# Optimization experiments

Hardware: AMD Instinct MI355X
Metric: run time of the kernel (lower is better)

The kernel has to match this reference:

```python
import jax, jax.numpy as jnp
import numpy as np

D_MODEL = 1024
NUM_HEADS = 16
D_K = D_MODEL // NUM_HEADS
D_FF = 4096
THETA = 10000.0
EPS = 1e-5


def rmsnorm(x, w):
    ms = jnp.mean(jnp.square(x), axis=-1, keepdims=True)
    return x * jax.lax.rsqrt(ms + EPS) * w


def rope(x, pos):
    # x: [B, H, S, d_k]; pos: [S]
    half = x.shape[-1] // 2
    inv_freq = THETA ** (-jnp.arange(half, dtype=x.dtype) * 2.0 / x.shape[-1])  # [half]
    ang = pos.astype(x.dtype)[:, None] * inv_freq[None, :]  # [S, half]
    cos, sin = jnp.cos(ang), jnp.sin(ang)
    xe, xo = x[..., 0::2], x[..., 1::2]
    oe = xe * cos - xo * sin
    oo = xe * sin + xo * cos
    return jnp.stack([oe, oo], axis=-1).reshape(x.shape)


def setup_inputs() -> dict:
    key = jax.random.key(0)
    ks = jax.random.split(key, 10)
    std_d = 1.0 / np.sqrt(D_MODEL)
    std_f = 1.0 / np.sqrt(D_FF)
    B, S = 4, 2048
    return {
        "x": jax.random.normal(ks[0], (B, S, D_MODEL), dtype=jnp.float32),
        "token_positions": jnp.arange(S, dtype=jnp.int32),
        "q_proj": jax.random.normal(ks[1], (D_MODEL, D_MODEL), dtype=jnp.float32) * std_d,
        "k_proj": jax.random.normal(ks[2], (D_MODEL, D_MODEL), dtype=jnp.float32) * std_d,
        "v_proj": jax.random.normal(ks[3], (D_MODEL, D_MODEL), dtype=jnp.float32) * std_d,
        "o_proj": jax.random.normal(ks[4], (D_MODEL, D_MODEL), dtype=jnp.float32) * std_d,
        "w1": jax.random.normal(ks[5], (D_FF, D_MODEL), dtype=jnp.float32) * std_d,
        "w2": jax.random.normal(ks[6], (D_MODEL, D_FF), dtype=jnp.float32) * std_f,
        "w3": jax.random.normal(ks[7], (D_FF, D_MODEL), dtype=jnp.float32) * std_d,
        "ln1_w": jnp.ones((D_MODEL,), dtype=jnp.float32),
        "ln2_w": jnp.ones((D_MODEL,), dtype=jnp.float32),
    }


def reference(x, token_positions, q_proj, k_proj, v_proj, o_proj, w1, w2, w3, ln1_w, ln2_w):
    B, S, _ = x.shape
    x_ln = rmsnorm(x, ln1_w)
    q = x_ln @ q_proj.T
    k = x_ln @ k_proj.T
    v = x_ln @ v_proj.T
    # [B, S, D] -> [B, H, S, d_k]
    def split_heads(t):
        return t.reshape(B, S, NUM_HEADS, D_K).transpose(0, 2, 1, 3)
    q, k, v = split_heads(q), split_heads(k), split_heads(v)
    q = rope(q, token_positions)
    k = rope(k, token_positions)
    scores = jnp.einsum("bhqd,bhkd->bhqk", q, k) / jnp.sqrt(jnp.asarray(D_K, x.dtype))
    causal = jnp.tril(jnp.ones((S, S), dtype=bool))
    scores = jnp.where(causal, scores, -jnp.inf)
    attn = jax.nn.softmax(scores, axis=-1)
    out = jnp.einsum("bhqk,bhkd->bhqd", attn, v)
    out = out.transpose(0, 2, 1, 3).reshape(B, S, D_MODEL)
    x = x + out @ o_proj.T
    x_ln2 = rmsnorm(x, ln2_w)
    u = x_ln2 @ w1.T
    vff = x_ln2 @ w3.T
    ff = (u * jax.nn.sigmoid(u)) * vff
    return x + ff @ w2.T
```

## Files before the change

kernel.cpp:

```cpp
#include <hip/hip_runtime.h>
#include <hip/hip_bf16.h>


typedef unsigned short u16;
typedef __attribute__((ext_vector_type(8))) short short8;
typedef __attribute__((ext_vector_type(4))) float f32x4;
typedef __attribute__((ext_vector_type(16))) float f32x16;

#define MFMA16(a, b, c) __builtin_amdgcn_mfma_f32_16x16x32_bf16(a, b, c, 0, 0, 0)
#define MFMA32(a, b, c) __builtin_amdgcn_mfma_f32_32x32x16_bf16(a, b, c, 0, 0, 0)
#define VMC(N) asm volatile("s_waitcnt vmcnt(" #N ")" ::: "memory")

__device__ __forceinline__ u16 f2b(float f) {
  union { float f; unsigned u; } x; x.f = f;
  unsigned r = x.u + 0x7FFFu + ((x.u >> 16) & 1u);
  return (u16)(r >> 16);
}
__device__ __forceinline__ float b2f(u16 h) {
  union { unsigned u; float f; } x; x.u = ((unsigned)h) << 16;
  return x.f;
}
__device__ __forceinline__ unsigned pkbf(float a, float b) {
  __hip_bfloat162 h = __float22bfloat162_rn(make_float2(a, b));
  union { __hip_bfloat162 h; unsigned u; } cv; cv.h = h;
  return cv.u;
}
__device__ __forceinline__ void async16(const void* g, void* l) {
  __builtin_amdgcn_global_load_lds(
      (const __attribute__((address_space(1))) void*)g,
      (__attribute__((address_space(3))) void*)l, 16, 0, 0);
}

template <int MODE>
__global__ __launch_bounds__(256, 2) void gemm_bt(
    const u16* __restrict__ A, const u16* __restrict__ B,
    u16* __restrict__ Cb, float* __restrict__ Cf, const float* __restrict__ R,
    int M, int N, int K) {
  __shared__ __align__(16) u16 As[128 * 64];
  __shared__ __align__(16) u16 Bs[128 * 64];
  const int tid = threadIdx.x;
  const int l = tid & 63, w = tid >> 6;
  const int wr = w & 1, wc = w >> 1;
  const int lr = l & 31, lh = l >> 5;
  const size_t m0 = (size_t)blockIdx.y * 128, n0 = (size_t)blockIdx.x * 128;
  f32x16 acc[2][2] = {};
  for (int k0 = 0; k0 < K; k0 += 64) {
#pragma unroll
    for (int t = 0; t < 4; ++t) {
      int c = t * 256 + tid;
      int r = c >> 3;
      int gc = ((c & 7) ^ (r & 7)) << 3;
      async16(A + (m0 + r) * (size_t)K + k0 + gc, &As[c * 8]);
    }
#pragma unroll
    for (int t = 0; t < 4; ++t) {
      int c = t * 256 + tid;
      int r = c >> 3;
      int gc = ((c & 7) ^ (r & 7)) << 3;
      async16(B + (n0 + r) * (size_t)K + k0 + gc, &Bs[c * 8]);
    }
    __syncthreads();
#pragma unroll
    for (int c = 0; c < 4; ++c) {
      const int c8 = c * 2 + lh;
      short8 af[2], bfr[2];
#pragma unroll
      for (int mi = 0; mi < 2; ++mi) {
        int r = wr * 64 + mi * 32 + lr;
        af[mi] = *(const short8*)&As[r * 64 + ((c8 ^ (r & 7)) << 3)];
      }
#pragma unroll
      for (int ni = 0; ni < 2; ++ni) {
        int r = wc * 64 + ni * 32 + lr;
        bfr[ni] = *(const short8*)&Bs[r * 64 + ((c8 ^ (r & 7)) << 3)];
      }
#pragma unroll
      for (int mi = 0; mi < 2; ++mi)
#pragma unroll
        for (int ni = 0; ni < 2; ++ni)
          acc[mi][ni] = MFMA32(af[mi], bfr[ni], acc[mi][ni]);
    }
    __syncthreads();
  }
#pragma unroll
  for (int mi = 0; mi < 2; ++mi)
#pragma unroll
    for (int ni = 0; ni < 2; ++ni) {
      size_t n = n0 + wc * 64 + ni * 32 + lr;
#pragma unroll
      for (int reg = 0; reg < 16; ++reg) {
        size_t m = m0 + wr * 64 + mi * 32 + (reg & 3) + 8 * (reg >> 2) + 4 * lh;
        float v = acc[mi][ni][reg];
        if (MODE == 0)
          Cb[m * (size_t)N + n] = f2b(v);
        else
          Cf[m * (size_t)N + n] = v + R[m * (size_t)N + n];
      }
    }
}

__global__ __launch_bounds__(256, 2) void ffn_gemm(
    const u16* __restrict__ A, const u16* __restrict__ B1,
    const u16* __restrict__ B3, u16* __restrict__ Hout, int M, int N, int K) {
  __shared__ __align__(16) u16 As[128 * 64];
  __shared__ __align__(16) u16 B1s[128 * 64];
  __shared__ __align__(16) u16 B3s[128 * 64];
  const int tid = threadIdx.x;
  const int l = tid & 63, w = tid >> 6;
  const int wr = w & 1, wc = w >> 1;
  const int lr = l & 31, lh = l >> 5;
  const size_t m0 = (size_t)blockIdx.y * 128, n0 = (size_t)blockIdx.x * 128;
  f32x16 a1[2][2] = {}, a3[2][2] = {};
  for (int k0 = 0; k0 < K; k0 += 64) {
#pragma unroll
    for (int t = 0; t < 4; ++t) {
      int c = t * 256 + tid;
      int r = c >> 3;
      int gc = ((c & 7) ^ (r & 7)) << 3;
      async16(A + (m0 + r) * (size_t)K + k0 + gc, &As[c * 8]);
      async16(B1 + (n0 + r) * (size_t)K + k0 + gc, &B1s[c * 8]);
      async16(B3 + (n0 + r) * (size_t)K + k0 + gc, &B3s[c * 8]);
    }
    __syncthreads();
#pragma unroll
    for (int c = 0; c < 4; ++c) {
      const int c8 = c * 2 + lh;
      short8 af[2], b1f[2], b3f[2];
#pragma unroll
      for (int mi = 0; mi < 2; ++mi) {
        int r = wr * 64 + mi * 32 + lr;
        af[mi] = *(const short8*)&As[r * 64 + ((c8 ^ (r & 7)) << 3)];
      }
#pragma unroll
      for (int ni = 0; ni < 2; ++ni) {
        int r = wc * 64 + ni * 32 + lr;
        b1f[ni] = *(const short8*)&B1s[r * 64 + ((c8 ^ (r & 7)) << 3)];
        b3f[ni] = *(const short8*)&B3s[r * 64 + ((c8 ^ (r & 7)) << 3)];
      }
#pragma unroll
      for (int mi = 0; mi < 2; ++mi)
#pragma unroll
        for (int ni = 0; ni < 2; ++ni) {
          a1[mi][ni] = MFMA32(af[mi], b1f[ni], a1[mi][ni]);
          a3[mi][ni] = MFMA32(af[mi], b3f[ni], a3[mi][ni]);
        }
    }
    __syncthreads();
  }
#pragma unroll
  for (int mi = 0; mi < 2; ++mi)
#pragma unroll
    for (int ni = 0; ni < 2; ++ni) {
      size_t n = n0 + wc * 64 + ni * 32 + lr;
#pragma unroll
      for (int reg = 0; reg < 16; ++reg) {
        size_t m = m0 + wr * 64 + mi * 32 + (reg & 3) + 8 * (reg >> 2) + 4 * lh;
        float u = a1[mi][ni][reg];
        float g = u / (1.0f + __expf(-u));
        Hout[m * (size_t)N + n] = f2b(g * a3[mi][ni][reg]);
      }
    }
}

__global__ __launch_bounds__(256, 2) void attn_k(
    const u16* __restrict__ qh, const u16* __restrict__ kh,
    const u16* __restrict__ vt, u16* __restrict__ aout) {
  __shared__ __align__(16) u16 Ks[128 * 64];
  __shared__ __align__(16) u16 Vs[64 * 128];
  __shared__ __align__(16) u16 Ps[128 * 136];
  const int tid = threadIdx.x;
  const int l = tid & 63, w = tid >> 6;
  const int q = l & 15, lq = l >> 4;
  const int bh = blockIdx.y;
  const size_t base = (size_t)bh * (2048 * 64);
  const int b = bh >> 4, h = bh & 15;

#define STAGE_K(kvt)                                                          \
  { _Pragma("unroll") for (int t = 0; t < 4; ++t) {                           \
      int p = t * 256 + tid;                                                  \
      int r = p >> 3, cs = p & 7;                                             \
      async16(kh + base + (size_t)((kvt) * 128 + r) * 64 + ((cs ^ (r & 7)) << 3), \
              &Ks[p * 8]); } }
#define STAGE_V(kvt)                                                          \
  { _Pragma("unroll") for (int t = 0; t < 4; ++t) {                           \
      int p = t * 256 + tid;                                                  \
      int r = p >> 4, cs = p & 15;                                            \
      async16(vt + base + (size_t)r * 2048 + (kvt) * 128 + ((cs ^ (r & 15)) << 3), \
              &Vs[p * 8]); } }
#define BARRIER                                                               \
  __builtin_amdgcn_sched_barrier(0);                                          \
  __builtin_amdgcn_s_barrier();                                               \
  __builtin_amdgcn_sched_barrier(0)

#pragma unroll 1
  for (int pass = 0; pass < 2; ++pass) {
    const int qt = pass ? (int)blockIdx.x : 15 - (int)blockIdx.x;
    const int q0 = qt << 7;
    const int nt = qt + 1;
    const int qcol[2] = {q0 + w * 16 + q, q0 + 64 + w * 16 + q};
    short8 bq[2][2];
#pragma unroll
    for (int sub = 0; sub < 2; ++sub)
#pragma unroll
      for (int kk = 0; kk < 2; ++kk)
        bq[sub][kk] = *(const short8*)(qh + base + (size_t)qcol[sub] * 64 + kk * 32 + lq * 8);

    f32x4 o[2][4] = {};
    float mI[2] = {-1e30f, -1e30f}, lI[2] = {0.0f, 0.0f};
    u16* pr0 = &Ps[(w * 16 + q) * 136];
    u16* pr1 = &Ps[(64 + w * 16 + q) * 136];

    BARRIER;
    STAGE_K(0);
    STAGE_V(0);

#pragma unroll 1
    for (int it = 0; it < nt; ++it) {
      if (it == 0) { VMC(4); } else { VMC(0); }
      BARRIER;
      if (it) STAGE_V(it);

      f32x4 s[2][8] = {};
#pragma unroll
      for (int kk = 0; kk < 2; ++kk) {
#pragma unroll
        for (int mt = 0; mt < 8; ++mt) {
          int row = mt * 16 + q;
          short8 ak = *(const short8*)&Ks[row * 64 + (((kk * 4 + lq) ^ (q & 7)) << 3)];
          s[0][mt] = MFMA16(ak, bq[0][kk], s[0][mt]);
          s[1][mt] = MFMA16(ak, bq[1][kk], s[1][mt]);
        }
      }
      BARRIER;
      if (it + 1 < nt) STAGE_K(it + 1);

      const bool last = (it == nt - 1);
      if (last) {
        const int kv0 = it << 7;
#pragma unroll
        for (int sub = 0; sub < 2; ++sub)
#pragma unroll
          for (int mt = 0; mt < 8; ++mt)
#pragma unroll
            for (int r = 0; r < 4; ++r)
              if (kv0 + mt * 16 + lq * 4 + r > qcol[sub]) s[sub][mt][r] = -1e30f;
      }
#pragma unroll
      for (int sub = 0; sub < 2; ++sub) {
        float tm[16];
#pragma unroll
        for (int i = 0; i < 16; ++i)
          tm[i] = fmaxf(s[sub][i >> 2][i & 3], s[sub][(i + 16) >> 2][(i + 16) & 3]);
#pragma unroll
        for (int i = 0; i < 8; ++i) tm[i] = fmaxf(tm[i], tm[i + 8]);
#pragma unroll
        for (int i = 0; i < 4; ++i) tm[i] = fmaxf(tm[i], tm[i + 4]);
        float mx = fmaxf(fmaxf(tm[0], tm[2]), fmaxf(tm[1], tm[3]));
        float mn = mI[sub];
        const bool full = !__all(mx <= mI[sub] + 8.0f);
        if (full) {
          mx = fmaxf(mx, __shfl_xor(mx, 16, 64));
          mx = fmaxf(mx, __shfl_xor(mx, 32, 64));
          mn = fmaxf(mI[sub], mx);
        }
        float ts[16];
#pragma unroll
        for (int i = 0; i < 16; ++i) {
          float pa = exp2f(s[sub][i >> 2][i & 3] - mn);
          float pb = exp2f(s[sub][(i + 16) >> 2][(i + 16) & 3] - mn);
          s[sub][i >> 2][i & 3] = pa;
          s[sub][(i + 16) >> 2][(i + 16) & 3] = pb;
          ts[i] = pa + pb;
        }
#pragma unroll
        for (int i = 0; i < 8; ++i) ts[i] += ts[i + 8];
#pragma unroll
        for (int i = 0; i < 4; ++i) ts[i] += ts[i + 4];
        float rs = (ts[0] + ts[2]) + (ts[1] + ts[3]);
        rs += __shfl_xor(rs, 16, 64);
        rs += __shfl_xor(rs, 32, 64);
        if (full) {
          const float al = exp2f(mI[sub] - mn);
          mI[sub] = mn;
          lI[sub] = lI[sub] * al + rs;
#pragma unroll
          for (int mt = 0; mt < 4; ++mt)
#pragma unroll
            for (int r = 0; r < 4; ++r) o[sub][mt][r] *= al;
        } else {
          lI[sub] += rs;
        }
        u16* pr = sub ? pr1 : pr0;
#pragma unroll
        for (int mt = 0; mt < 8; ++mt) {
          uint2 pd;
          pd.x = pkbf(s[sub][mt][0], s[sub][mt][1]);
          pd.y = pkbf(s[sub][mt][2], s[sub][mt][3]);
          *(uint2*)&pr[mt * 16 + lq * 4] = pd;
        }
      }
      if (it + 1 < nt) { VMC(4); } else { VMC(0); }
      BARRIER;
#pragma unroll
      for (int kk = 0; kk < 4; ++kk) {
        short8 bp0 = *(const short8*)&pr0[kk * 32 + lq * 8];
        short8 bp1 = *(const short8*)&pr1[kk * 32 + lq * 8];
#pragma unroll
        for (int mt = 0; mt < 4; ++mt) {
          int row = mt * 16 + q;
          short8 av = *(const short8*)&Vs[row * 128 + (((kk * 4 + lq) ^ (row & 15)) << 3)];
          o[0][mt] = MFMA16(av, bp0, o[0][mt]);
          o[1][mt] = MFMA16(av, bp1, o[1][mt]);
        }
      }
    }
#pragma unroll
    for (int sub = 0; sub < 2; ++sub) {
      const float inv = 1.0f / lI[sub];
#pragma unroll
      for (int mt = 0; mt < 4; ++mt) {
        uint2 pd;
        pd.x = pkbf(o[sub][mt][0] * inv, o[sub][mt][1] * inv);
        pd.y = pkbf(o[sub][mt][2] * inv, o[sub][mt][3] * inv);
        *(uint2*)&aout[((size_t)(b * 2048 + qcol[sub])) * 1024 + h * 64 + mt * 16 + lq * 4] = pd;
      }
    }
  }
#undef STAGE_K
#undef STAGE_V
#undef BARRIER
}

__global__ __launch_bounds__(256) void rmsnorm_k(
    const float* __restrict__ x, const float* __restrict__ w, u16* __restrict__ out) {
  const int row = blockIdx.x;
  const int tid = threadIdx.x;
  const float4 v = ((const float4*)(x + (size_t)row * 1024))[tid];
  float ss = v.x * v.x + v.y * v.y + v.z * v.z + v.w * v.w;
#pragma unroll
  for (int d = 1; d < 64; d <<= 1) ss += __shfl_xor(ss, d, 64);
  __shared__ float red[4];
  if ((tid & 63) == 0) red[tid >> 6] = ss;
  __syncthreads();
  const float sc = rsqrtf((red[0] + red[1] + red[2] + red[3]) * (1.0f / 1024.0f) + 1e-5f);
  const float4 wv = ((const float4*)w)[tid];
  uint2 pv;
  pv.x = pkbf(v.x * sc * wv.x, v.y * sc * wv.y);
  pv.y = pkbf(v.z * sc * wv.z, v.w * sc * wv.w);
  *(uint2*)(out + (size_t)row * 1024 + tid * 4) = pv;
}

__global__ __launch_bounds__(256) void rope_k(
    const u16* __restrict__ qkv, u16* __restrict__ qh, u16* __restrict__ kh,
    const int* __restrict__ pos) {
  int idx = blockIdx.x * 256 + threadIdx.x;
  int grp = idx & 255;
  int row = idx >> 8;
  int which = grp >> 7;
  int p = grp & 127;
  int s = row & 2047, b = row >> 11;
  int h = p >> 3, gi = p & 7;
  const u16* src = qkv + (size_t)row * 3072 + which * 1024 + h * 64 + gi * 8;
  uint4 in = *(const uint4*)src;
  const u16* e = (const u16*)&in;
  const float fp = (float)pos[s];
  const float scale = which ? 1.0f : 0.18033688011112042f;
  uint4 outv;
  unsigned* ov = (unsigned*)&outv;
#pragma unroll
  for (int j = 0; j < 4; ++j) {
    int i = gi * 4 + j;
    float xe = b2f(e[2 * j]), xo = b2f(e[2 * j + 1]);
    float inv = exp2f(-(float)(2 * i) * (13.287712379549449f / 64.0f));
    float ang = fp * inv;
    float sn, cs;
    __sincosf(ang, &sn, &cs);
    ov[j] = pkbf((xe * cs - xo * sn) * scale, (xe * sn + xo * cs) * scale);
  }
  u16* dst = (which ? kh : qh) + (((size_t)(b * 16 + h)) * 2048 + s) * 64 + gi * 8;
  *(uint4*)dst = outv;
}

__global__ __launch_bounds__(256) void transv_k(
    const u16* __restrict__ qkv, u16* __restrict__ vt) {
  __shared__ u16 t[64][65];
  const int bh = blockIdx.y, s0 = blockIdx.x * 64;
  const int b = bh >> 4, h = bh & 15;
  const int tid = threadIdx.x;
#pragma unroll
  for (int i = 0; i < 16; ++i) {
    int e = i * 256 + tid;
    int sl = e >> 6, d = e & 63;
    t[sl][d] = qkv[((size_t)(b * 2048 + s0 + sl)) * 3072 + 2048 + h * 64 + d];
  }
  __syncthreads();
#pragma unroll
  for (int i = 0; i < 16; ++i) {
    int e = i * 256 + tid;
    int d = e >> 6, sl = e & 63;
    vt[((size_t)(bh * 64 + d)) * 2048 + s0 + sl] = t[sl][d];
  }
}

__global__ __launch_bounds__(256) void cvt_all(
    const float* __restrict__ qp, const float* __restrict__ kp,
    const float* __restrict__ vp, const float* __restrict__ op,
    const float* __restrict__ w1, const float* __restrict__ w3,
    const float* __restrict__ w2,
    u16* __restrict__ WQKV, u16* __restrict__ WO,
    u16* __restrict__ W1, u16* __restrict__ W3, u16* __restrict__ W2) {
  int i = blockIdx.x * 256 + threadIdx.x;
  const float* src;
  u16* dst;
  int off;
  if (i < 1048576) {
    int seg = i >> 18, within = i & 262143;
    src = (seg == 0) ? qp : (seg == 1) ? kp : (seg == 2) ? vp : op;
    dst = (seg == 3) ? WO : WQKV + (size_t)seg * 1048576;
    off = within;
  } else {
    int j = i - 1048576;
    int seg = j >> 20;
    off = j & 1048575;
    src = (seg == 0) ? w1 : (seg == 1) ? w3 : w2;
    dst = (seg == 0) ? W1 : (seg == 1) ? W3 : W2;
  }
  float4 v = ((const float4*)src)[off];
  uint2 pv;
  pv.x = pkbf(v.x, v.y);
  pv.y = pkbf(v.z, v.w);
  *(uint2*)(dst + (size_t)off * 4) = pv;
}

extern "C" void kernel_launch(void* const* d_in, const int* in_sizes, int n_in,
                              void* d_out, int out_size, void* d_ws, size_t ws_size,
                              hipStream_t stream) {
  const float* x   = (const float*)d_in[0];
  const int*   pos = (const int*)d_in[1];
  const float* qp  = (const float*)d_in[2];
  const float* kp  = (const float*)d_in[3];
  const float* vp  = (const float*)d_in[4];
  const float* op  = (const float*)d_in[5];
  const float* w1  = (const float*)d_in[6];
  const float* w2  = (const float*)d_in[7];
  const float* w3  = (const float*)d_in[8];
  const float* ln1 = (const float*)d_in[9];
  const float* ln2 = (const float*)d_in[10];
  float* out = (float*)d_out;
  char* ws = (char*)d_ws;
  const size_t MB = 1024 * 1024;

  u16* WQKV = (u16*)(ws + 0 * MB);
  u16* WO   = (u16*)(ws + 6 * MB);
  u16* W1   = (u16*)(ws + 8 * MB);
  u16* W3   = (u16*)(ws + 16 * MB);
  u16* W2   = (u16*)(ws + 24 * MB);
  u16* XLN  = (u16*)(ws + 32 * MB);
  u16* QKV  = (u16*)(ws + 48 * MB);
  u16* QH   = (u16*)(ws + 96 * MB);
  u16* KH   = (u16*)(ws + 112 * MB);
  u16* VT   = (u16*)(ws + 128 * MB);
  u16* ATT  = (u16*)(ws + 48 * MB);
  u16* XLN2 = (u16*)(ws + 64 * MB);
  u16* Hbuf = (u16*)(ws + 80 * MB);
  (void)in_sizes; (void)n_in; (void)out_size; (void)ws_size;

  cvt_all<<<16384, 256, 0, stream>>>(qp, kp, vp, op, w1, w3, w2,
                                     WQKV, WO, W1, W3, W2);
  rmsnorm_k<<<8192, 256, 0, stream>>>(x, ln1, XLN);
  gemm_bt<0><<<dim3(24, 64), 256, 0, stream>>>(XLN, WQKV, QKV, nullptr, nullptr, 8192, 3072, 1024);
  rope_k<<<8192, 256, 0, stream>>>(QKV, QH, KH, pos);
  transv_k<<<dim3(32, 64), 256, 0, stream>>>(QKV, VT);
  attn_k<<<dim3(8, 64), 256, 0, stream>>>(QH, KH, VT, ATT);
  gemm_bt<1><<<dim3(8, 64), 256, 0, stream>>>(ATT, WO, nullptr, out, x, 8192, 1024, 1024);
  rmsnorm_k<<<8192, 256, 0, stream>>>(out, ln2, XLN2);
  ffn_gemm<<<dim3(32, 64), 256, 0, stream>>>(XLN2, W1, W3, Hbuf, 8192, 4096, 1024);
  gemm_bt<1><<<dim3(8, 64), 256, 0, stream>>>(Hbuf, W2, nullptr, out, out, 8192, 1024, 4096);
}
```

Baseline: 575.3 us.

## Raise occupancy for gemm and attention, halve P buffer, merge small prep kernels

Raises the launch-bounds occupancy hint from 2 to 3 for the GEMM and attention kernels. Attention now writes P through a single half-size LDS buffer, one sub-tile at a time, so LDS use fits more blocks per CU. The softmax max and sum reductions are rewritten as per-lane chains. Weight conversion is fused with the first RMSNorm, and RoPE is fused with the V transpose, which saves two launches. The lower register budget may cause spills, and reusing one P buffer across sub-tiles risks a write-after-read hazard without an extra barrier.

```diff
diff --git a/kernel.cpp b/kernel.cpp
--- a/kernel.cpp
+++ b/kernel.cpp
@@ -32,7 +32,7 @@
 }
 
 template <int MODE>
-__global__ __launch_bounds__(256, 2) void gemm_bt(
+__global__ __launch_bounds__(256, 3) void gemm_bt(
     const u16* __restrict__ A, const u16* __restrict__ B,
     u16* __restrict__ Cb, float* __restrict__ Cf, const float* __restrict__ R,
     int M, int N, int K) {
@@ -162,12 +162,12 @@
     }
 }
 
-__global__ __launch_bounds__(256, 2) void attn_k(
+__global__ __launch_bounds__(256, 3) void attn_k(
     const u16* __restrict__ qh, const u16* __restrict__ kh,
     const u16* __restrict__ vt, u16* __restrict__ aout) {
   __shared__ __align__(16) u16 Ks[128 * 64];
   __shared__ __align__(16) u16 Vs[64 * 128];
-  __shared__ __align__(16) u16 Ps[128 * 136];
+  __shared__ __align__(16) u16 Ps[64 * 136];
   const int tid = threadIdx.x;
   const int l = tid & 63, w = tid >> 6;
   const int q = l & 15, lq = l >> 4;
@@ -207,8 +207,7 @@
 
     f32x4 o[2][4] = {};
     float mI[2] = {-1e30f, -1e30f}, lI[2] = {0.0f, 0.0f};
-    u16* pr0 = &Ps[(w * 16 + q) * 136];
-    u16* pr1 = &Ps[(64 + w * 16 + q) * 136];
+    u16* pr = &Ps[(w * 16 + q) * 136];
 
     BARRIER;
     STAGE_K(0);
@@ -247,15 +246,15 @@
       }
 #pragma unroll
       for (int sub = 0; sub < 2; ++sub) {
-        float tm[16];
-#pragma unroll
-        for (int i = 0; i < 16; ++i)
-          tm[i] = fmaxf(s[sub][i >> 2][i & 3], s[sub][(i + 16) >> 2][(i + 16) & 3]);
-#pragma unroll
-        for (int i = 0; i < 8; ++i) tm[i] = fmaxf(tm[i], tm[i + 8]);
-#pragma unroll
-        for (int i = 0; i < 4; ++i) tm[i] = fmaxf(tm[i], tm[i + 4]);
-        float mx = fmaxf(fmaxf(tm[0], tm[2]), fmaxf(tm[1], tm[3]));
+        float c0 = -1e30f, c1 = -1e30f, c2 = -1e30f, c3 = -1e30f;
+#pragma unroll
+        for (int mt = 0; mt < 8; ++mt) {
+          c0 = fmaxf(c0, s[sub][mt][0]);
+          c1 = fmaxf(c1, s[sub][mt][1]);
+          c2 = fmaxf(c2, s[sub][mt][2]);
+          c3 = fmaxf(c3, s[sub][mt][3]);
+        }
+        float mx = fmaxf(fmaxf(c0, c1), fmaxf(c2, c3));
         float mn = mI[sub];
         const bool full = !__all(mx <= mI[sub] + 8.0f);
         if (full) {
@@ -263,20 +262,18 @@
           mx = fmaxf(mx, __shfl_xor(mx, 32, 64));
           mn = fmaxf(mI[sub], mx);
         }
-        float ts[16];
-#pragma unroll
-        for (int i = 0; i < 16; ++i) {
-          float pa = exp2f(s[sub][i >> 2][i & 3] - mn);
-          float pb = exp2f(s[sub][(i + 16) >> 2][(i + 16) & 3] - mn);
-          s[sub][i >> 2][i & 3] = pa;
-          s[sub][(i + 16) >> 2][(i + 16) & 3] = pb;
-          ts[i] = pa + pb;
-        }
-#pragma unroll
-        for (int i = 0; i < 8; ++i) ts[i] += ts[i + 8];
-#pragma unroll
-        for (int i = 0; i < 4; ++i) ts[i] += ts[i + 4];
-        float rs = (ts[0] + ts[2]) + (ts[1] + ts[3]);
+        float t0 = 0.0f, t1 = 0.0f, t2 = 0.0f, t3 = 0.0f;
+#pragma unroll
+        for (int mt = 0; mt < 8; ++mt) {
+          float p0 = exp2f(s[sub][mt][0] - mn);
+          float p1 = exp2f(s[sub][mt][1] - mn);
+          float p2 = exp2f(s[sub][mt][2] - mn);
+          float p3 = exp2f(s[sub][mt][3] - mn);
+          s[sub][mt][0] = p0; s[sub][mt][1] = p1;
+          s[sub][mt][2] = p2; s[sub][mt][3] = p3;
+          t0 += p0; t1 += p1; t2 += p2; t3 += p3;
+        }
+        float rs = (t0 + t1) + (t2 + t3);
         rs += __shfl_xor(rs, 16, 64);
         rs += __shfl_xor(rs, 32, 64);
         if (full) {
@@ -290,7 +287,11 @@
         } else {
           lI[sub] += rs;
         }
-        u16* pr = sub ? pr1 : pr0;
+      }
+      if (it + 1 < nt) { VMC(4); } else { VMC(0); }
+      BARRIER;
+#pragma unroll
+      for (int sub = 0; sub < 2; ++sub) {
 #pragma unroll
         for (int mt = 0; mt < 8; ++mt) {
           uint2 pd;
@@ -298,19 +299,15 @@
           pd.y = pkbf(s[sub][mt][2], s[sub][mt][3]);
           *(uint2*)&pr[mt * 16 + lq * 4] = pd;
         }
-      }
-      if (it + 1 < nt) { VMC(4); } else { VMC(0); }
-      BARRIER;
-#pragma unroll
-      for (int kk = 0; kk < 4; ++kk) {
-        short8 bp0 = *(const short8*)&pr0[kk * 32 + lq * 8];
-        short8 bp1 = *(const short8*)&pr1[kk * 32 + lq * 8];
-#pragma unroll
-        for (int mt = 0; mt < 4; ++mt) {
-          int row = mt * 16 + q;
-          short8 av = *(const short8*)&Vs[row * 128 + (((kk * 4 + lq) ^ (row & 15)) << 3)];
-          o[0][mt] = MFMA16(av, bp0, o[0][mt]);
-          o[1][mt] = MFMA16(av, bp1, o[1][mt]);
+#pragma unroll
+        for (int kk = 0; kk < 4; ++kk) {
+          short8 bp = *(const short8*)&pr[kk * 32 + lq * 8];
+#pragma unroll
+          for (int mt = 0; mt < 4; ++mt) {
+            int row = mt * 16 + q;
+            short8 av = *(const short8*)&Vs[row * 128 + (((kk * 4 + lq) ^ (row & 15)) << 3)];
+            o[sub][mt] = MFMA16(av, bp, o[sub][mt]);
+          }
         }
       }
     }
@@ -329,6 +326,56 @@
 #undef STAGE_K
 #undef STAGE_V
 #undef BARRIER
+}
+
+__global__ __launch_bounds__(256) void prep_k(
+    const float* __restrict__ x, const float* __restrict__ ln1, u16* __restrict__ xout,
+    const float* __restrict__ qp, const float* __restrict__ kp,
+    const float* __restrict__ vp, const float* __restrict__ op,
+    const float* __restrict__ w1, const float* __restrict__ w3,
+    const float* __restrict__ w2,
+    u16* __restrict__ WQKV, u16* __restrict__ WO,
+    u16* __restrict__ W1, u16* __restrict__ W3, u16* __restrict__ W2) {
+  __shared__ float red[4];
+  const int bid = blockIdx.x;
+  const int tid = threadIdx.x;
+  if (bid < 8192) {
+    const int row = bid;
+    const float4 v = ((const float4*)(x + (size_t)row * 1024))[tid];
+    float ss = v.x * v.x + v.y * v.y + v.z * v.z + v.w * v.w;
+#pragma unroll
+    for (int d = 1; d < 64; d <<= 1) ss += __shfl_xor(ss, d, 64);
+    if ((tid & 63) == 0) red[tid >> 6] = ss;
+    __syncthreads();
+    const float sc = rsqrtf((red[0] + red[1] + red[2] + red[3]) * (1.0f / 1024.0f) + 1e-5f);
+    const float4 wv = ((const float4*)ln1)[tid];
+    uint2 pv;
+    pv.x = pkbf(v.x * sc * wv.x, v.y * sc * wv.y);
+    pv.y = pkbf(v.z * sc * wv.z, v.w * sc * wv.w);
+    *(uint2*)(xout + (size_t)row * 1024 + tid * 4) = pv;
+  } else {
+    int i = (bid - 8192) * 256 + tid;
+    const float* src;
+    u16* dst;
+    int off;
+    if (i < 1048576) {
+      int seg = i >> 18, within = i & 262143;
+      src = (seg == 0) ? qp : (seg == 1) ? kp : (seg == 2) ? vp : op;
+      dst = (seg == 3) ? WO : WQKV + (size_t)seg * 1048576;
+      off = within;
+    } else {
+      int j = i - 1048576;
+      int seg = j >> 20;
+      off = j & 1048575;
+      src = (seg == 0) ? w1 : (seg == 1) ? w3 : w2;
+      dst = (seg == 0) ? W1 : (seg == 1) ? W3 : W2;
+    }
+    float4 v = ((const float4*)src)[off];
+    uint2 pv;
+    pv.x = pkbf(v.x, v.y);
+    pv.y = pkbf(v.z, v.w);
+    *(uint2*)(dst + (size_t)off * 4) = pv;
+  }
 }
 
 __global__ __launch_bounds__(256) void rmsnorm_k(
@@ -350,86 +397,57 @@
   *(uint2*)(out + (size_t)row * 1024 + tid * 4) = pv;
 }
 
-__global__ __launch_bounds__(256) void rope_k(
+__global__ __launch_bounds__(256) void rope_tv(
     const u16* __restrict__ qkv, u16* __restrict__ qh, u16* __restrict__ kh,
-    const int* __restrict__ pos) {
-  int idx = blockIdx.x * 256 + threadIdx.x;
-  int grp = idx & 255;
-  int row = idx >> 8;
-  int which = grp >> 7;
-  int p = grp & 127;
-  int s = row & 2047, b = row >> 11;
-  int h = p >> 3, gi = p & 7;
-  const u16* src = qkv + (size_t)row * 3072 + which * 1024 + h * 64 + gi * 8;
-  uint4 in = *(const uint4*)src;
-  const u16* e = (const u16*)&in;
-  const float fp = (float)pos[s];
-  const float scale = which ? 1.0f : 0.18033688011112042f;
-  uint4 outv;
-  unsigned* ov = (unsigned*)&outv;
-#pragma unroll
-  for (int j = 0; j < 4; ++j) {
-    int i = gi * 4 + j;
-    float xe = b2f(e[2 * j]), xo = b2f(e[2 * j + 1]);
-    float inv = exp2f(-(float)(2 * i) * (13.287712379549449f / 64.0f));
-    float ang = fp * inv;
-    float sn, cs;
-    __sincosf(ang, &sn, &cs);
-    ov[j] = pkbf((xe * cs - xo * sn) * scale, (xe * sn + xo * cs) * scale);
+    const int* __restrict__ pos, u16* __restrict__ vt) {
+  __shared__ u16 t[64][65];
+  const int bid = blockIdx.x;
+  const int tid = threadIdx.x;
+  if (bid < 8192) {
+    int idx = bid * 256 + tid;
+    int grp = idx & 255;
+    int row = idx >> 8;
+    int which = grp >> 7;
+    int p = grp & 127;
+    int s = row & 2047, b = row >> 11;
+    int h = p >> 3, gi = p & 7;
+    const u16* src = qkv + (size_t)row * 3072 + which * 1024 + h * 64 + gi * 8;
+    uint4 in = *(const uint4*)src;
+    const u16* e = (const u16*)&in;
+    const float fp = (float)pos[s];
+    const float scale = which ? 1.0f : 0.18033688011112042f;
+    uint4 outv;
+    unsigned* ov = (unsigned*)&outv;
+#pragma unroll
+    for (int j = 0; j < 4; ++j) {
+      int i = gi * 4 + j;
+      float xe = b2f(e[2 * j]), xo = b2f(e[2 * j + 1]);
+      float inv = exp2f(-(float)(2 * i) * (13.287712379549449f / 64.0f));
+      float ang = fp * inv;
+      float sn, cs;
+      __sincosf(ang, &sn, &cs);
+      ov[j] = pkbf((xe * cs - xo * sn) * scale, (xe * sn + xo * cs) * scale);
+    }
+    u16* dst = (which ? kh : qh) + (((size_t)(b * 16 + h)) * 2048 + s) * 64 + gi * 8;
+    *(uint4*)dst = outv;
+  } else {
+    const int bq = bid - 8192;
+    const int s0 = (bq & 31) * 64, bh = bq >> 5;
+    const int b = bh >> 4, h = bh & 15;
+#pragma unroll
+    for (int i = 0; i < 16; ++i) {
+      int e = i * 256 + tid;
+      int sl = e >> 6, d = e & 63;
+      t[sl][d] = qkv[((size_t)(b * 2048 + s0 + sl)) * 3072 + 2048 + h * 64 + d];
+    }
+    __syncthreads();
+#pragma unroll
+    for (int i = 0; i < 16; ++i) {
+      int e = i * 256 + tid;
+      int d = e >> 6, sl = e & 63;
+      vt[((size_t)(bh * 64 + d)) * 2048 + s0 + sl] = t[sl][d];
+    }
   }
-  u16* dst = (which ? kh : qh) + (((size_t)(b * 16 + h)) * 2048 + s) * 64 + gi * 8;
-  *(uint4*)dst = outv;
-}
-
-__global__ __launch_bounds__(256) void transv_k(
-    const u16* __restrict__ qkv, u16* __restrict__ vt) {
-  __shared__ u16 t[64][65];
-  const int bh = blockIdx.y, s0 = blockIdx.x * 64;
-  const int b = bh >> 4, h = bh & 15;
-  const int tid = threadIdx.x;
-#pragma unroll
-  for (int i = 0; i < 16; ++i) {
-    int e = i * 256 + tid;
-    int sl = e >> 6, d = e & 63;
-    t[sl][d] = qkv[((size_t)(b * 2048 + s0 + sl)) * 3072 + 2048 + h * 64 + d];
-  }
-  __syncthreads();
-#pragma unroll
-  for (int i = 0; i < 16; ++i) {
-    int e = i * 256 + tid;
-    int d = e >> 6, sl = e & 63;
-    vt[((size_t)(bh * 64 + d)) * 2048 + s0 + sl] = t[sl][d];
-  }
-}
-
-__global__ __launch_bounds__(256) void cvt_all(
-    const float* __restrict__ qp, const float* __restrict__ kp,
-    const float* __restrict__ vp, const float* __restrict__ op,
-    const float* __restrict__ w1, const float* __restrict__ w3,
-    const float* __restrict__ w2,
-    u16* __restrict__ WQKV, u16* __restrict__ WO,
-    u16* __restrict__ W1, u16* __restrict__ W3, u16* __restrict__ W2) {
-  int i = blockIdx.x * 256 + threadIdx.x;
-  const float* src;
-  u16* dst;
-  int off;
-  if (i < 1048576) {
-    int seg = i >> 18, within = i & 262143;
-    src = (seg == 0) ? qp : (seg == 1) ? kp : (seg == 2) ? vp : op;
-    dst = (seg == 3) ? WO : WQKV + (size_t)seg * 1048576;
-    off = within;
-  } else {
-    int j = i - 1048576;
-    int seg = j >> 20;
-    off = j & 1048575;
-    src = (seg == 0) ? w1 : (seg == 1) ? w3 : w2;
-    dst = (seg == 0) ? W1 : (seg == 1) ? W3 : W2;
-  }
-  float4 v = ((const float4*)src)[off];
-  uint2 pv;
-  pv.x = pkbf(v.x, v.y);
-  pv.y = pkbf(v.z, v.w);
-  *(uint2*)(dst + (size_t)off * 4) = pv;
 }
 
 extern "C" void kernel_launch(void* const* d_in, const int* in_sizes, int n_in,
@@ -465,12 +483,10 @@
   u16* Hbuf = (u16*)(ws + 80 * MB);
   (void)in_sizes; (void)n_in; (void)out_size; (void)ws_size;
 
-  cvt_all<<<16384, 256, 0, stream>>>(qp, kp, vp, op, w1, w3, w2,
-                                     WQKV, WO, W1, W3, W2);
-  rmsnorm_k<<<8192, 256, 0, stream>>>(x, ln1, XLN);
+  prep_k<<<24576, 256, 0, stream>>>(x, ln1, XLN, qp, kp, vp, op, w1, w3, w2,
+                                    WQKV, WO, W1, W3, W2);
   gemm_bt<0><<<dim3(24, 64), 256, 0, stream>>>(XLN, WQKV, QKV, nullptr, nullptr, 8192, 3072, 1024);
-  rope_k<<<8192, 256, 0, stream>>>(QKV, QH, KH, pos);
-  transv_k<<<dim3(32, 64), 256, 0, stream>>>(QKV, VT);
+  rope_tv<<<10240, 256, 0, stream>>>(QKV, QH, KH, pos, VT);
   attn_k<<<dim3(8, 64), 256, 0, stream>>>(QH, KH, VT, ATT);
   gemm_bt<1><<<dim3(8, 64), 256, 0, stream>>>(ATT, WO, nullptr, out, x, 8192, 1024, 1024);
   rmsnorm_k<<<8192, 256, 0, stream>>>(out, ln2, XLN2);
```

Result: slower. 677.0 us (+17.7%).
